# Performance work log

Measured on AMD Instinct MI355X. Metric: run time of the kernel, lower is better.

The kernel has to match this reference:

```python
import jax, jax.numpy as jnp
import numpy as np

B, L = 2048, 128          # (src,tgt) pairs x walk positions
K = 4                     # num_layers + 1
ENC = 108                 # enc_dim
D2, D3, D4 = 172, 512, 172
NKEYS = 1_000_000         # unique (batch,node,time,sign) keys in nodetime2emb_maps


def setup_inputs() -> dict:
    key = jax.random.key(0)
    ks = jax.random.split(key, 8)
    emb_table = jax.random.uniform(ks[0], (NKEYS, 2, K), dtype=jnp.float32)
    idx = jax.random.randint(ks[1], (B, L), 0, NKEYS, dtype=jnp.int32)
    W1 = jax.random.normal(ks[2], (K, ENC), dtype=jnp.float32) * (1.0 / np.sqrt(K))
    b1 = jnp.zeros((ENC,), dtype=jnp.float32)
    W2 = jax.random.normal(ks[3], (ENC, ENC), dtype=jnp.float32) * (1.0 / np.sqrt(ENC))
    b2 = jnp.zeros((ENC,), dtype=jnp.float32)
    x2 = jax.random.normal(ks[4], (B, L, D2), dtype=jnp.float32)
    fc1_w = jax.random.normal(ks[5], (ENC + D2, D3), dtype=jnp.float32) * (1.0 / np.sqrt(ENC + D2))
    fc1_b = jnp.zeros((D3,), dtype=jnp.float32)
    fc2_w = jax.random.normal(ks[6], (D3, D4), dtype=jnp.float32) * (1.0 / np.sqrt(D3))
    fc2_b = jnp.zeros((D4,), dtype=jnp.float32)
    return {"emb_table": emb_table, "idx": idx, "W1": W1, "b1": b1, "W2": W2,
            "b2": b2, "x2": x2, "fc1_w": fc1_w, "fc1_b": fc1_b,
            "fc2_w": fc2_w, "fc2_b": fc2_b}


def reference(emb_table, idx, W1, b1, W2, b2, x2, fc1_w, fc1_b, fc2_w, fc2_b):
    # --- PositionEncoder.forward: gather per-(node,time) encodings [B,L,2,K]
    enc = emb_table[idx]
    # --- get_trainable_encodings: Linear(K->ENC), ReLU, Linear(ENC->ENC), sum over src/tgt axis
    h = jax.nn.relu(jnp.einsum('blsk,ke->blse', enc, W1) + b1)
    h = jnp.einsum('blse,ef->blsf', h, W2) + b2
    pe = h.sum(axis=-2)                      # [B, L, ENC]
    # --- MergeLayer (edge_embedding_type='concat'): concat + fc1 + ReLU + fc2
    x = jnp.concatenate([pe, x2], axis=-1)   # [B, L, ENC + D2]
    z = jax.nn.relu(x @ fc1_w + fc1_b) @ fc2_w + fc2_b  # [B, L, D4]
    return z
```

## Files before the change

kernel.cpp:

```cpp
#include <hip/hip_runtime.h>
#include <stdint.h>

typedef __bf16 bf16x8 __attribute__((ext_vector_type(8)));
typedef float  f32x4  __attribute__((ext_vector_type(4)));
typedef unsigned short u16x4 __attribute__((ext_vector_type(4)));

#define XS_B   592
#define HS_B   1040
#define B1_OFF 75776
#define B1_SZ  32768
#define B2_OFF 133120
#define B2_SZ  12288
#define LDS_SZ 157696

#define WS_FC1T   0
#define WS_FC2T   294912
#define WS_BIAS   491520

__device__ __forceinline__ unsigned short f2bf(float f) {
  union { float f; unsigned u; } c; c.f = f;
  unsigned u = c.u;
  u += 0x7FFFu + ((u >> 16) & 1u);
  return (unsigned short)(u >> 16);
}

__device__ __forceinline__ void g2l16(const void* g, void* l) {
  __builtin_amdgcn_global_load_lds(
      (const __attribute__((address_space(1))) void*)g,
      (__attribute__((address_space(3))) void*)l, 16, 0, 0);
}

__global__ void POLAR_prep_fc1(const float* __restrict__ W2,
                               const float* __restrict__ fc1_w,
                               const float* __restrict__ fc1_b,
                               const float* __restrict__ b2,
                               unsigned short* __restrict__ fc1t,
                               float* __restrict__ bias_eff) {
  int n = blockIdx.x;
  int k = threadIdx.x;
  float v = 0.f;
  if (k < 108) {
    for (int f = 0; f < 108; ++f) v += W2[k*108 + f] * fc1_w[f*512 + n];
  } else if (k < 280) {
    v = fc1_w[k*512 + n];
  }
  fc1t[n*288 + k] = f2bf(v);
  if (k == 0) {
    float bb = fc1_b[n];
    for (int f = 0; f < 108; ++f) bb += 2.f * b2[f] * fc1_w[f*512 + n];
    bias_eff[n] = bb;
  }
}

__global__ void POLAR_prep_fc2(const float* __restrict__ fc2_w,
                               unsigned short* __restrict__ fc2t) {
  int n = blockIdx.x;
  int k = threadIdx.x;
  float v = (n < 172) ? fc2_w[k*172 + n] : 0.f;
  fc2t[n*512 + k] = f2bf(v);
}

__global__ __launch_bounds__(512, 2) void POLAR_fused(
    const float* __restrict__ emb, const int* __restrict__ idx,
    const float* __restrict__ W1, const float* __restrict__ b1,
    const float* __restrict__ x2,
    const unsigned short* __restrict__ fc1t,
    const float* __restrict__ bias_eff,
    const unsigned short* __restrict__ fc2t,
    const float* __restrict__ fc2b,
    float* __restrict__ out)
{
  __shared__ __attribute__((aligned(16))) char smem[LDS_SZ];
  const int tid  = threadIdx.x;
  const int lane = tid & 63;
  const int w    = tid >> 6;
  const int wm   = w >> 2;
  const int wn   = w & 3;
  const int blk  = blockIdx.x;
  const int l15  = lane & 15;
  const int l4   = lane >> 4;

  {
    int nr = lane >> 2, slds = lane & 3;
    #pragma unroll
    for (int j = 0; j < 4; ++j) {
      int c = w * 4 + j;
      int n = c * 16 + nr;
      int sg = slds ^ ((n >> 1) & 3);
      g2l16((const char*)fc1t + n * 576 + sg * 16, smem + B1_OFF + c * 1024);
    }
  }

  {
    int r  = tid >> 2;
    int li = tid & 3;
    size_t g = (size_t)blk * 128 + r;
    int key = idx[g];
    const float* ep = emb + (size_t)key * 8;
    f32x4 e0 = *(const f32x4*)ep;
    f32x4 e1 = *(const f32x4*)(ep + 4);
    int ebase = li * 27;
    for (int t = 0; t < 27; ++t) {
      int e = ebase + t;
      float w0 = W1[e], w1v = W1[108 + e], w2v = W1[216 + e], w3v = W1[324 + e];
      float bb = b1[e];
      float a0 = fmaxf(e0.x*w0 + e0.y*w1v + e0.z*w2v + e0.w*w3v + bb, 0.f);
      float a1 = fmaxf(e1.x*w0 + e1.y*w1v + e1.z*w2v + e1.w*w3v + bb, 0.f);
      *(unsigned short*)(smem + r * XS_B + e * 2) = f2bf(a0 + a1);
    }
  }

  {
    const f32x4* x2v = (const f32x4*)(x2 + (size_t)blk * 128 * 172);
    for (int t = tid; t < 128 * 43; t += 512) {
      int r = t / 43, c4 = t - r * 43;
      f32x4 v = x2v[r * 43 + c4];
      u16x4 s; s.x = f2bf(v.x); s.y = f2bf(v.y); s.z = f2bf(v.z); s.w = f2bf(v.w);
      *(u16x4*)(smem + r * XS_B + 216 + c4 * 8) = s;
    }
    if (tid < 128) {
      u16x4 z = (u16x4){0,0,0,0};
      *(u16x4*)(smem + tid * XS_B + 560) = z;
      *(u16x4*)(smem + tid * XS_B + 568) = z;
    }
  }
  __syncthreads();

  f32x4 acc[4][8];
  #pragma unroll
  for (int i = 0; i < 4; ++i)
    #pragma unroll
    for (int j = 0; j < 8; ++j)
      acc[i][j] = (f32x4){0.f, 0.f, 0.f, 0.f};

  #pragma unroll 1
  for (int kt = 0; kt < 9; ++kt) {
    int cur = kt & 1;
    if (kt < 8) {
      int nr = lane >> 2, slds = lane & 3;
      char* dst = smem + B1_OFF + (cur ^ 1) * B1_SZ;
      #pragma unroll
      for (int j = 0; j < 4; ++j) {
        int c = w * 4 + j;
        int n = c * 16 + nr;
        int sg = slds ^ ((n >> 1) & 3);
        g2l16((const char*)fc1t + n * 576 + (kt + 1) * 64 + sg * 16, dst + c * 1024);
      }
    }
    bf16x8 af[4];
    #pragma unroll
    for (int i = 0; i < 4; ++i) {
      int r = wm * 64 + i * 16 + l15;
      af[i] = *(const bf16x8*)(smem + r * XS_B + kt * 64 + l4 * 16);
    }
    const char* bb = smem + B1_OFF + cur * B1_SZ;
    bf16x8 bv[8];
    #pragma unroll
    for (int j = 0; j < 8; ++j) {
      int n = wn * 128 + j * 16 + l15;
      int so = l4 ^ ((n >> 1) & 3);
      bv[j] = *(const bf16x8*)(bb + n * 64 + so * 16);
    }
    #pragma unroll
    for (int i = 0; i < 4; ++i)
      #pragma unroll
      for (int j = 0; j < 8; ++j)
        acc[i][j] = __builtin_amdgcn_mfma_f32_16x16x32_bf16(af[i], bv[j], acc[i][j], 0, 0, 0);
    __syncthreads();
  }

  {
    int nr = lane >> 2, slds = lane & 3;
    for (int c = w; c < 12; c += 8) {
      int n = c * 16 + nr;
      int sg = slds ^ ((n >> 1) & 3);
      g2l16((const char*)fc2t + n * 1024 + sg * 16, smem + B2_OFF + c * 1024);
    }
  }

  #pragma unroll
  for (int j = 0; j < 8; ++j) {
    int col = wn * 128 + j * 16 + l15;
    float be = bias_eff[col];
    #pragma unroll
    for (int i = 0; i < 4; ++i) {
      #pragma unroll
      for (int r2 = 0; r2 < 4; ++r2) {
        int row = wm * 64 + i * 16 + l4 * 4 + r2;
        float v = fmaxf(acc[i][j][r2] + be, 0.f);
        *(unsigned short*)(smem + row * HS_B + col * 2) = f2bf(v);
      }
    }
  }
  __syncthreads();

  f32x4 acc2[4][3];
  #pragma unroll
  for (int i = 0; i < 4; ++i)
    #pragma unroll
    for (int j = 0; j < 3; ++j)
      acc2[i][j] = (f32x4){0.f, 0.f, 0.f, 0.f};

  #pragma unroll 1
  for (int kt = 0; kt < 16; ++kt) {
    int cur = kt & 1;
    if (kt < 15) {
      int nr = lane >> 2, slds = lane & 3;
      char* dst = smem + B2_OFF + (cur ^ 1) * B2_SZ;
      for (int c = w; c < 12; c += 8) {
        int n = c * 16 + nr;
        int sg = slds ^ ((n >> 1) & 3);
        g2l16((const char*)fc2t + n * 1024 + (kt + 1) * 64 + sg * 16, dst + c * 1024);
      }
    }
    bf16x8 af[4];
    #pragma unroll
    for (int i = 0; i < 4; ++i) {
      int r = wm * 64 + i * 16 + l15;
      af[i] = *(const bf16x8*)(smem + r * HS_B + kt * 64 + l4 * 16);
    }
    const char* bb2 = smem + B2_OFF + cur * B2_SZ;
    bf16x8 bv[3];
    #pragma unroll
    for (int j = 0; j < 3; ++j) {
      int n = wn * 48 + j * 16 + l15;
      int so = l4 ^ ((n >> 1) & 3);
      bv[j] = *(const bf16x8*)(bb2 + n * 64 + so * 16);
    }
    #pragma unroll
    for (int i = 0; i < 4; ++i)
      #pragma unroll
      for (int j = 0; j < 3; ++j)
        acc2[i][j] = __builtin_amdgcn_mfma_f32_16x16x32_bf16(af[i], bv[j], acc2[i][j], 0, 0, 0);
    __syncthreads();
  }

  const size_t orow0 = (size_t)blk * 128;
  #pragma unroll
  for (int j = 0; j < 3; ++j) {
    int col = wn * 48 + j * 16 + l15;
    if (col < 172) {
      float bias = fc2b[col];
      #pragma unroll
      for (int i = 0; i < 4; ++i) {
        #pragma unroll
        for (int r2 = 0; r2 < 4; ++r2) {
          int row = wm * 64 + i * 16 + l4 * 4 + r2;
          out[(orow0 + row) * 172 + col] = acc2[i][j][r2] + bias;
        }
      }
    }
  }
}

extern "C" void kernel_launch(void* const* d_in, const int* in_sizes, int n_in,
                              void* d_out, int out_size, void* d_ws, size_t ws_size,
                              hipStream_t stream) {
  (void)in_sizes; (void)n_in; (void)out_size; (void)ws_size;
  const float* emb   = (const float*)d_in[0];
  const int*   idx   = (const int*)d_in[1];
  const float* W1    = (const float*)d_in[2];
  const float* b1    = (const float*)d_in[3];
  const float* W2    = (const float*)d_in[4];
  const float* b2    = (const float*)d_in[5];
  const float* x2    = (const float*)d_in[6];
  const float* fc1_w = (const float*)d_in[7];
  const float* fc1_b = (const float*)d_in[8];
  const float* fc2_w = (const float*)d_in[9];
  const float* fc2_b = (const float*)d_in[10];
  float* out = (float*)d_out;
  char* ws = (char*)d_ws;
  unsigned short* fc1t = (unsigned short*)(ws + WS_FC1T);
  unsigned short* fc2t = (unsigned short*)(ws + WS_FC2T);
  float* bias_eff = (float*)(ws + WS_BIAS);

  POLAR_prep_fc1<<<512, 288, 0, stream>>>(W2, fc1_w, fc1_b, b2, fc1t, bias_eff);
  POLAR_prep_fc2<<<192, 512, 0, stream>>>(fc2_w, fc2t);
  POLAR_fused<<<2048, 512, 0, stream>>>(emb, idx, W1, b1, x2, fc1t, bias_eff,
                                        fc2t, fc2_b, out);
}
```

Baseline: 305.4 us.

## Use 1024-thread blocks, read weights directly from global, swizzle LDS activations

The fused kernel now launches 1024 threads (16 waves) per block with smaller per-wave tiles. Weight tiles for fc1 and fc2 are no longer staged into LDS with global_load_lds double buffering; each wave reads its B fragments straight from global memory and relies on cache. LDS holds only the activations, laid out with an XOR swizzle instead of padded rows. The hidden-layer writeback pairs values across lanes with shuffles to store 32-bit words. The aim is to cut LDS footprint and per-iteration barriers and to raise occupancy, at the cost of repeated global/L2 weight reads from every wave.

```diff
diff --git a/kernel.cpp b/kernel.cpp
--- a/kernel.cpp
+++ b/kernel.cpp
@@ -5,13 +5,9 @@
 typedef float  f32x4  __attribute__((ext_vector_type(4)));
 typedef unsigned short u16x4 __attribute__((ext_vector_type(4)));
 
-#define XS_B   592
-#define HS_B   1040
-#define B1_OFF 75776
-#define B1_SZ  32768
-#define B2_OFF 133120
-#define B2_SZ  12288
-#define LDS_SZ 157696
+#define XROW_B 576
+#define HROW_B 1024
+#define LDS_SZ 131072
 
 #define WS_FC1T   0
 #define WS_FC2T   294912
@@ -22,12 +18,6 @@
   unsigned u = c.u;
   u += 0x7FFFu + ((u >> 16) & 1u);
   return (unsigned short)(u >> 16);
-}
-
-__device__ __forceinline__ void g2l16(const void* g, void* l) {
-  __builtin_amdgcn_global_load_lds(
-      (const __attribute__((address_space(1))) void*)g,
-      (__attribute__((address_space(3))) void*)l, 16, 0, 0);
 }
 
 __global__ void POLAR_prep_fc1(const float* __restrict__ W2,
@@ -60,7 +50,7 @@
   fc2t[n*512 + k] = f2bf(v);
 }
 
-__global__ __launch_bounds__(512, 2) void POLAR_fused(
+__global__ __launch_bounds__(1024, 4) void POLAR_fused(
     const float* __restrict__ emb, const int* __restrict__ idx,
     const float* __restrict__ W1, const float* __restrict__ b1,
     const float* __restrict__ x2,
@@ -74,178 +64,158 @@
   const int tid  = threadIdx.x;
   const int lane = tid & 63;
   const int w    = tid >> 6;
-  const int wm   = w >> 2;
-  const int wn   = w & 3;
   const int blk  = blockIdx.x;
   const int l15  = lane & 15;
   const int l4   = lane >> 4;
 
   {
-    int nr = lane >> 2, slds = lane & 3;
-    #pragma unroll
-    for (int j = 0; j < 4; ++j) {
-      int c = w * 4 + j;
-      int n = c * 16 + nr;
-      int sg = slds ^ ((n >> 1) & 3);
-      g2l16((const char*)fc1t + n * 576 + sg * 16, smem + B1_OFF + c * 1024);
-    }
-  }
-
-  {
-    int r  = tid >> 2;
-    int li = tid & 3;
-    size_t g = (size_t)blk * 128 + r;
-    int key = idx[g];
+    int r  = tid >> 3;
+    int li = tid & 7;
+    int key = idx[(size_t)blk * 128 + r];
     const float* ep = emb + (size_t)key * 8;
     f32x4 e0 = *(const f32x4*)ep;
     f32x4 e1 = *(const f32x4*)(ep + 4);
-    int ebase = li * 27;
-    for (int t = 0; t < 27; ++t) {
-      int e = ebase + t;
+    unsigned sw = ((unsigned)(r >> 1) & 3u) << 4;
+    for (int e = li; e < 108; e += 8) {
       float w0 = W1[e], w1v = W1[108 + e], w2v = W1[216 + e], w3v = W1[324 + e];
       float bb = b1[e];
       float a0 = fmaxf(e0.x*w0 + e0.y*w1v + e0.z*w2v + e0.w*w3v + bb, 0.f);
       float a1 = fmaxf(e1.x*w0 + e1.y*w1v + e1.z*w2v + e1.w*w3v + bb, 0.f);
-      *(unsigned short*)(smem + r * XS_B + e * 2) = f2bf(a0 + a1);
+      *(unsigned short*)(smem + r * XROW_B + ((unsigned)(2*e) ^ sw)) = f2bf(a0 + a1);
     }
   }
 
   {
     const f32x4* x2v = (const f32x4*)(x2 + (size_t)blk * 128 * 172);
-    for (int t = tid; t < 128 * 43; t += 512) {
+    #pragma unroll 1
+    for (int t = tid; t < 128 * 43; t += 1024) {
       int r = t / 43, c4 = t - r * 43;
-      f32x4 v = x2v[r * 43 + c4];
+      f32x4 v = x2v[t];
       u16x4 s; s.x = f2bf(v.x); s.y = f2bf(v.y); s.z = f2bf(v.z); s.w = f2bf(v.w);
-      *(u16x4*)(smem + r * XS_B + 216 + c4 * 8) = s;
+      unsigned be = 216u + 8u * (unsigned)c4;
+      unsigned sw = ((unsigned)(r >> 1) & 3u) << 4;
+      *(u16x4*)(smem + r * XROW_B + (be ^ sw)) = s;
     }
     if (tid < 128) {
-      u16x4 z = (u16x4){0,0,0,0};
-      *(u16x4*)(smem + tid * XS_B + 560) = z;
-      *(u16x4*)(smem + tid * XS_B + 568) = z;
+      unsigned sw = ((unsigned)(tid >> 1) & 3u) << 4;
+      union { long2 l; } z; z.l.x = 0; z.l.y = 0;
+      *(long2*)(smem + tid * XROW_B + (560u ^ sw)) = z.l;
     }
   }
   __syncthreads();
 
-  f32x4 acc[4][8];
+  const int wm = w >> 3;
+  const int wn = w & 7;
+  f32x4 acc[4][4];
   #pragma unroll
   for (int i = 0; i < 4; ++i)
     #pragma unroll
-    for (int j = 0; j < 8; ++j)
+    for (int j = 0; j < 4; ++j)
       acc[i][j] = (f32x4){0.f, 0.f, 0.f, 0.f};
 
+  const char* fb1 = (const char*)fc1t;
   #pragma unroll 1
   for (int kt = 0; kt < 9; ++kt) {
-    int cur = kt & 1;
-    if (kt < 8) {
-      int nr = lane >> 2, slds = lane & 3;
-      char* dst = smem + B1_OFF + (cur ^ 1) * B1_SZ;
+    bf16x8 af[4], bv[4];
+    #pragma unroll
+    for (int i = 0; i < 4; ++i) {
+      int row = wm * 64 + i * 16 + l15;
+      unsigned off = ((unsigned)(kt * 64 + l4 * 16)) ^ ((((unsigned)row >> 1) & 3u) << 4);
+      af[i] = *(const bf16x8*)(smem + row * XROW_B + off);
+    }
+    #pragma unroll
+    for (int j = 0; j < 4; ++j) {
+      int n = wn * 64 + j * 16 + l15;
+      bv[j] = *(const bf16x8*)(fb1 + n * 576 + kt * 64 + l4 * 16);
+    }
+    #pragma unroll
+    for (int i = 0; i < 4; ++i)
+      #pragma unroll
+      for (int j = 0; j < 4; ++j)
+        acc[i][j] = __builtin_amdgcn_mfma_f32_16x16x32_bf16(af[i], bv[j], acc[i][j], 0, 0, 0);
+  }
+  __syncthreads();
+
+  {
+    const int odd = lane & 1;
+    #pragma unroll
+    for (int i = 0; i < 4; ++i) {
       #pragma unroll
       for (int j = 0; j < 4; ++j) {
-        int c = w * 4 + j;
-        int n = c * 16 + nr;
-        int sg = slds ^ ((n >> 1) & 3);
-        g2l16((const char*)fc1t + n * 576 + (kt + 1) * 64 + sg * 16, dst + c * 1024);
+        int col0 = wn * 64 + j * 16 + l15;
+        float be = bias_eff[col0];
+        float a0 = fmaxf(acc[i][j][0] + be, 0.f);
+        float a1 = fmaxf(acc[i][j][1] + be, 0.f);
+        float a2 = fmaxf(acc[i][j][2] + be, 0.f);
+        float a3 = fmaxf(acc[i][j][3] + be, 0.f);
+        float t0 = odd ? a0 : a2;
+        float t1 = odd ? a1 : a3;
+        float p0 = __shfl_xor(t0, 1);
+        float p1 = __shfl_xor(t1, 1);
+        unsigned w0 = odd ? ((unsigned)f2bf(p0) | ((unsigned)f2bf(a2) << 16))
+                          : ((unsigned)f2bf(a0) | ((unsigned)f2bf(p0) << 16));
+        unsigned w1 = odd ? ((unsigned)f2bf(p1) | ((unsigned)f2bf(a3) << 16))
+                          : ((unsigned)f2bf(a1) | ((unsigned)f2bf(p1) << 16));
+        int row0 = wm * 64 + i * 16 + l4 * 4 + (odd ? 2 : 0);
+        int row1 = row0 + 1;
+        unsigned cb = (unsigned)((col0 & ~1) * 2);
+        *(unsigned*)(smem + row0 * HROW_B + (cb ^ (((unsigned)row0 & 7u) << 4))) = w0;
+        *(unsigned*)(smem + row1 * HROW_B + (cb ^ (((unsigned)row1 & 7u) << 4))) = w1;
       }
     }
-    bf16x8 af[4];
-    #pragma unroll
-    for (int i = 0; i < 4; ++i) {
-      int r = wm * 64 + i * 16 + l15;
-      af[i] = *(const bf16x8*)(smem + r * XS_B + kt * 64 + l4 * 16);
-    }
-    const char* bb = smem + B1_OFF + cur * B1_SZ;
-    bf16x8 bv[8];
-    #pragma unroll
-    for (int j = 0; j < 8; ++j) {
-      int n = wn * 128 + j * 16 + l15;
-      int so = l4 ^ ((n >> 1) & 3);
-      bv[j] = *(const bf16x8*)(bb + n * 64 + so * 16);
-    }
-    #pragma unroll
-    for (int i = 0; i < 4; ++i)
-      #pragma unroll
-      for (int j = 0; j < 8; ++j)
-        acc[i][j] = __builtin_amdgcn_mfma_f32_16x16x32_bf16(af[i], bv[j], acc[i][j], 0, 0, 0);
-    __syncthreads();
-  }
-
-  {
-    int nr = lane >> 2, slds = lane & 3;
-    for (int c = w; c < 12; c += 8) {
-      int n = c * 16 + nr;
-      int sg = slds ^ ((n >> 1) & 3);
-      g2l16((const char*)fc2t + n * 1024 + sg * 16, smem + B2_OFF + c * 1024);
-    }
-  }
-
+  }
+  __syncthreads();
+
+  const int wm4 = w >> 2;
+  const int wn4 = w & 3;
+  f32x4 acc2[2][3];
   #pragma unroll
-  for (int j = 0; j < 8; ++j) {
-    int col = wn * 128 + j * 16 + l15;
-    float be = bias_eff[col];
-    #pragma unroll
-    for (int i = 0; i < 4; ++i) {
-      #pragma unroll
-      for (int r2 = 0; r2 < 4; ++r2) {
-        int row = wm * 64 + i * 16 + l4 * 4 + r2;
-        float v = fmaxf(acc[i][j][r2] + be, 0.f);
-        *(unsigned short*)(smem + row * HS_B + col * 2) = f2bf(v);
-      }
-    }
-  }
-  __syncthreads();
-
-  f32x4 acc2[4][3];
-  #pragma unroll
-  for (int i = 0; i < 4; ++i)
+  for (int i = 0; i < 2; ++i)
     #pragma unroll
     for (int j = 0; j < 3; ++j)
       acc2[i][j] = (f32x4){0.f, 0.f, 0.f, 0.f};
 
+  const char* fb2 = (const char*)fc2t;
   #pragma unroll 1
-  for (int kt = 0; kt < 16; ++kt) {
-    int cur = kt & 1;
-    if (kt < 15) {
-      int nr = lane >> 2, slds = lane & 3;
-      char* dst = smem + B2_OFF + (cur ^ 1) * B2_SZ;
-      for (int c = w; c < 12; c += 8) {
-        int n = c * 16 + nr;
-        int sg = slds ^ ((n >> 1) & 3);
-        g2l16((const char*)fc2t + n * 1024 + (kt + 1) * 64 + sg * 16, dst + c * 1024);
+  for (int kt = 0; kt < 8; ++kt) {
+    bf16x8 a2[2][2], b2v[3][2];
+    #pragma unroll
+    for (int i = 0; i < 2; ++i) {
+      int row = wm4 * 32 + i * 16 + l15;
+      unsigned swr = (((unsigned)row & 7u) << 4);
+      #pragma unroll
+      for (int s = 0; s < 2; ++s) {
+        unsigned off = ((unsigned)(kt * 128 + s * 64 + l4 * 16)) ^ swr;
+        a2[i][s] = *(const bf16x8*)(smem + row * HROW_B + off);
       }
     }
-    bf16x8 af[4];
-    #pragma unroll
-    for (int i = 0; i < 4; ++i) {
-      int r = wm * 64 + i * 16 + l15;
-      af[i] = *(const bf16x8*)(smem + r * HS_B + kt * 64 + l4 * 16);
-    }
-    const char* bb2 = smem + B2_OFF + cur * B2_SZ;
-    bf16x8 bv[3];
     #pragma unroll
     for (int j = 0; j < 3; ++j) {
-      int n = wn * 48 + j * 16 + l15;
-      int so = l4 ^ ((n >> 1) & 3);
-      bv[j] = *(const bf16x8*)(bb2 + n * 64 + so * 16);
-    }
-    #pragma unroll
-    for (int i = 0; i < 4; ++i)
-      #pragma unroll
-      for (int j = 0; j < 3; ++j)
-        acc2[i][j] = __builtin_amdgcn_mfma_f32_16x16x32_bf16(af[i], bv[j], acc2[i][j], 0, 0, 0);
-    __syncthreads();
+      int n = wn4 * 48 + j * 16 + l15;
+      #pragma unroll
+      for (int s = 0; s < 2; ++s)
+        b2v[j][s] = *(const bf16x8*)(fb2 + n * 1024 + kt * 128 + s * 64 + l4 * 16);
+    }
+    #pragma unroll
+    for (int s = 0; s < 2; ++s)
+      #pragma unroll
+      for (int i = 0; i < 2; ++i)
+        #pragma unroll
+        for (int j = 0; j < 3; ++j)
+          acc2[i][j] = __builtin_amdgcn_mfma_f32_16x16x32_bf16(a2[i][s], b2v[j][s], acc2[i][j], 0, 0, 0);
   }
 
   const size_t orow0 = (size_t)blk * 128;
   #pragma unroll
   for (int j = 0; j < 3; ++j) {
-    int col = wn * 48 + j * 16 + l15;
+    int col = wn4 * 48 + j * 16 + l15;
     if (col < 172) {
       float bias = fc2b[col];
       #pragma unroll
-      for (int i = 0; i < 4; ++i) {
+      for (int i = 0; i < 2; ++i) {
         #pragma unroll
         for (int r2 = 0; r2 < 4; ++r2) {
-          int row = wm * 64 + i * 16 + l4 * 4 + r2;
+          int row = wm4 * 32 + i * 16 + l4 * 4 + r2;
           out[(orow0 + row) * 172 + col] = acc2[i][j][r2] + bias;
         }
       }
@@ -276,6 +246,6 @@
 
   POLAR_prep_fc1<<<512, 288, 0, stream>>>(W2, fc1_w, fc1_b, b2, fc1t, bias_eff);
   POLAR_prep_fc2<<<192, 512, 0, stream>>>(fc2_w, fc2t);
-  POLAR_fused<<<2048, 512, 0, stream>>>(emb, idx, W1, b1, x2, fc1t, bias_eff,
-                                        fc2t, fc2_b, out);
-}
+  POLAR_fused<<<2048, 1024, 0, stream>>>(emb, idx, W1, b1, x2, fc1t, bias_eff,
+                                         fc2t, fc2_b, out);
+}
```

Result: slower. 405.7 us (+32.8%).
